# Optimization experiments

Measured on AMD Instinct MI355X. Metric: run time of the kernel, lower is better.

## Reference

```python
import jax, jax.numpy as jnp
import numpy as np

H = 16  # num heads
DH = 64  # head dim


def setup_inputs() -> dict:
    key = jax.random.key(0)
    ks = jax.random.split(key, 9)
    d = 1024
    s = 0.02
    return {
        "hidden_states": jax.random.normal(ks[0], (16, 1024, d), jnp.float32),
        "Wq": jax.random.normal(ks[1], (d, d), jnp.float32) * s,
        "bq": jax.random.normal(ks[2], (d,), jnp.float32) * s,
        "Wk": jax.random.normal(ks[3], (d, d), jnp.float32) * s,
        "bk": jax.random.normal(ks[4], (d,), jnp.float32) * s,
        "Wv": jax.random.normal(ks[5], (d, d), jnp.float32) * s,
        "bv": jax.random.normal(ks[6], (d,), jnp.float32) * s,
        "Wo": jax.random.normal(ks[7], (d, d), jnp.float32) * s,
        "bo": jax.random.normal(ks[8], (d,), jnp.float32) * s,
    }


def _heads(x):
    b, s, _ = x.shape
    return x.reshape(b, s, H, DH).transpose(0, 2, 1, 3)  # [B,H,S,Dh]


def reference(hidden_states, Wq, bq, Wk, bk, Wv, bv, Wo, bo):
    # torch nn.Linear: y = x @ W.T + b; weights here are [out, in]
    q = _heads(hidden_states @ Wq.T + bq)
    k = _heads(hidden_states @ Wk.T + bk)
    v = _heads(hidden_states @ Wv.T + bv)
    scores = jnp.einsum("bhqd,bhkd->bhqk", q, k) / jnp.sqrt(jnp.float32(DH))
    probs = jax.nn.softmax(scores, axis=-1)
    ctx = jnp.einsum("bhqk,bhkd->bhqd", probs, v)
    b, _, s, _ = ctx.shape
    ctx = ctx.transpose(0, 2, 1, 3).reshape(b, s, H * DH)
    out = ctx @ Wo.T + bo
    # module returns (attention_output, weights=None); return array only
    return out
```

## Files before the change

kernel.cpp:

```cpp
#include <hip/hip_runtime.h>
#include <hip/hip_bf16.h>
#include <stdint.h>


typedef short bf16x8 __attribute__((ext_vector_type(8)));
typedef float f32x4 __attribute__((ext_vector_type(4)));
typedef unsigned short ushort_t;
typedef ushort_t us8 __attribute__((ext_vector_type(8)));

__device__ __forceinline__ ushort_t f2b(float f) {
    unsigned x;
    __builtin_memcpy(&x, &f, 4);
    unsigned r = (x + 0x7fffu + ((x >> 16) & 1u)) >> 16;
    return (ushort_t)r;
}

__device__ __forceinline__ void glds16(const void* g, void* l) {
    __builtin_amdgcn_global_load_lds(
        (const __attribute__((address_space(1))) void*)g,
        (__attribute__((address_space(3))) void*)l, 16, 0, 0);
}

#define MFMA16(a, b, c) __builtin_amdgcn_mfma_f32_16x16x32_bf16((a), (b), (c), 0, 0, 0)

__global__ __launch_bounds__(256, 8) void cvt4_kernel(
    const float* __restrict__ s0, const float* __restrict__ s1,
    const float* __restrict__ s2, const float* __restrict__ s3,
    ushort_t* __restrict__ d0, ushort_t* __restrict__ d1,
    ushort_t* __restrict__ d2, ushort_t* __restrict__ d3, int n8)
{
    const float* in = (blockIdx.y == 0) ? s0 : (blockIdx.y == 1) ? s1
                       : (blockIdx.y == 2) ? s2 : s3;
    ushort_t* out = (blockIdx.y == 0) ? d0 : (blockIdx.y == 1) ? d1
                       : (blockIdx.y == 2) ? d2 : d3;
    int i = blockIdx.x * 256 + threadIdx.x;
    if (i >= n8) return;
    const float4* p = (const float4*)in + (size_t)i * 2;
    float4 a = p[0], b = p[1];
    us8 v;
    v[0] = f2b(a.x); v[1] = f2b(a.y); v[2] = f2b(a.z); v[3] = f2b(a.w);
    v[4] = f2b(b.x); v[5] = f2b(b.y); v[6] = f2b(b.z); v[7] = f2b(b.w);
    *((us8*)out + i) = v;
}

__global__ __launch_bounds__(256, 8) void cvt1_kernel(
    const float* __restrict__ in, ushort_t* __restrict__ out, int n8)
{
    int i = blockIdx.x * 256 + threadIdx.x;
    if (i >= n8) return;
    const float4* p = (const float4*)in + (size_t)i * 2;
    float4 a = p[0], b = p[1];
    us8 v;
    v[0] = f2b(a.x); v[1] = f2b(a.y); v[2] = f2b(a.z); v[3] = f2b(a.w);
    v[4] = f2b(b.x); v[5] = f2b(b.y); v[6] = f2b(b.z); v[7] = f2b(b.w);
    *((us8*)out + i) = v;
}

template <bool OUTF>
__global__ __launch_bounds__(512) void gemm256_kernel(
    const ushort_t* __restrict__ A,
    const ushort_t* __restrict__ W0, const ushort_t* __restrict__ W1, const ushort_t* __restrict__ W2,
    const float* __restrict__ b0, const float* __restrict__ b1, const float* __restrict__ b2,
    void* __restrict__ C0, void* __restrict__ C1, void* __restrict__ C2,
    float s0, float s1, float s2, int N, int K)
{
    const ushort_t* W = (blockIdx.z == 0) ? W0 : ((blockIdx.z == 1) ? W1 : W2);
    const float* bias = (blockIdx.z == 0) ? b0 : ((blockIdx.z == 1) ? b1 : b2);
    void* C = (blockIdx.z == 0) ? C0 : ((blockIdx.z == 1) ? C1 : C2);
    const float scale = (blockIdx.z == 0) ? s0 : ((blockIdx.z == 1) ? s1 : s2);

    __shared__ ushort_t lds[2][4][256 * 32];

    const int tid = threadIdx.x;
    const int lane = tid & 63;
    const int wave = tid >> 6;
    const int wr = wave >> 2;
    const int wc = wave & 3;
    const int rl = lane & 15;
    const int ck = lane >> 4;

    const int gx = gridDim.x;
    const int flat = blockIdx.y * gx + blockIdx.x;
    const int cpx = (gx * gridDim.y) >> 3;
    const int swz = (flat & 7) * cpx + (flat >> 3);
    const int bm = (swz % gx) * 256;
    const int bn = (swz / gx) * 256;

    const ushort_t* Ag = A + (size_t)bm * K;
    const ushort_t* Bg = W + (size_t)bn * K;

    const int q0 = tid, q1 = 512 + tid;
    const int sr0 = q0 >> 2, sc0 = (q0 & 3) * 8;
    const int sr1 = q1 >> 2, sc1 = (q1 & 3) * 8;

#define STG(gbase, kcol, dst) do { \
    glds16((gbase) + (size_t)sr0 * K + (kcol) + sc0, (dst) + q0 * 8); \
    glds16((gbase) + (size_t)sr1 * K + (kcol) + sc1, (dst) + q1 * 8); } while (0)

#define BARRIER() do { \
    __builtin_amdgcn_sched_barrier(0); \
    asm volatile("s_barrier" ::: "memory"); \
    __builtin_amdgcn_sched_barrier(0); } while (0)

#define VMCNT(n) asm volatile("s_waitcnt vmcnt(" #n ")" ::: "memory")

    f32x4 acc[8][4] = {};
    bf16x8 af[8], bfr[2];

    const int aoff = (wr * 128 + rl) * 32 + ck * 8;
    const int boff = (wc * 64 + rl) * 32 + ck * 8;

#define LDA(buf, kh) do { _Pragma("unroll") \
    for (int mi = 0; mi < 8; ++mi) \
        af[mi] = *(const bf16x8*)(&lds[buf][kh][0] + aoff + mi * 512); } while (0)
#define LDB(buf, kh, nb) do { \
    bfr[0] = *(const bf16x8*)(&lds[buf][2 + (kh)][0] + boff + (nb) * 1024); \
    bfr[1] = *(const bf16x8*)(&lds[buf][2 + (kh)][0] + boff + (nb) * 1024 + 512); } while (0)
#define MM(nb) do { __builtin_amdgcn_s_setprio(1); _Pragma("unroll") \
    for (int mi = 0; mi < 8; ++mi) { \
        acc[mi][2*(nb)]   = MFMA16(af[mi], bfr[0], acc[mi][2*(nb)]); \
        acc[mi][2*(nb)+1] = MFMA16(af[mi], bfr[1], acc[mi][2*(nb)+1]); } \
    __builtin_amdgcn_s_setprio(0); } while (0)

    STG(Ag, 0,  &lds[0][0][0]);
    STG(Bg, 0,  &lds[0][2][0]);
    STG(Ag, 32, &lds[0][1][0]);
    STG(Bg, 32, &lds[0][3][0]);
    STG(Ag, 64, &lds[1][0][0]);
    STG(Bg, 64, &lds[1][2][0]);
    VMCNT(4);
    BARRIER();

#pragma unroll 1
    for (int i = 0; i < 7; ++i) {
        const int t = 2 * i;
        const int kc1 = (t + 1) * 64, kc2 = (t + 2) * 64, kc3 = (t + 3) * 64;
        LDA(0, 0); LDB(0, 0, 0);
        STG(Ag, kc1 + 32, &lds[1][1][0]);
        BARRIER(); MM(0); BARRIER();
        LDB(0, 0, 1);
        STG(Bg, kc1 + 32, &lds[1][3][0]);
        BARRIER(); MM(1); BARRIER();
        LDA(0, 1); LDB(0, 1, 0);
        STG(Ag, kc2, &lds[0][0][0]);
        BARRIER(); MM(0); BARRIER();
        LDB(0, 1, 1);
        STG(Bg, kc2, &lds[0][2][0]);
        VMCNT(4);
        BARRIER(); MM(1); BARRIER();
        LDA(1, 0); LDB(1, 0, 0);
        STG(Ag, kc2 + 32, &lds[0][1][0]);
        BARRIER(); MM(0); BARRIER();
        LDB(1, 0, 1);
        STG(Bg, kc2 + 32, &lds[0][3][0]);
        BARRIER(); MM(1); BARRIER();
        LDA(1, 1); LDB(1, 1, 0);
        STG(Ag, kc3, &lds[1][0][0]);
        BARRIER(); MM(0); BARRIER();
        LDB(1, 1, 1);
        STG(Bg, kc3, &lds[1][2][0]);
        VMCNT(4);
        BARRIER(); MM(1); BARRIER();
    }

    {
        const int kc15 = 15 * 64;
        LDA(0, 0); LDB(0, 0, 0);
        STG(Ag, kc15 + 32, &lds[1][1][0]);
        BARRIER(); MM(0); BARRIER();
        LDB(0, 0, 1);
        STG(Bg, kc15 + 32, &lds[1][3][0]);
        BARRIER(); MM(1); BARRIER();
        LDA(0, 1); LDB(0, 1, 0);
        BARRIER(); MM(0); BARRIER();
        LDB(0, 1, 1);
        VMCNT(0);
        BARRIER(); MM(1); BARRIER();
        LDA(1, 0); LDB(1, 0, 0); MM(0);
        LDB(1, 0, 1); MM(1);
        LDA(1, 1); LDB(1, 1, 0); MM(0);
        LDB(1, 1, 1); MM(1);
    }

#pragma unroll
    for (int ni = 0; ni < 4; ++ni) {
        const int col = bn + wc * 64 + ni * 16 + rl;
        const float bv = bias[col];
#pragma unroll
        for (int mi = 0; mi < 8; ++mi) {
            const int rbase = bm + wr * 128 + mi * 16 + ck * 4;
#pragma unroll
            for (int r = 0; r < 4; ++r) {
                float v = (acc[mi][ni][r] + bv) * scale;
                if (OUTF)
                    ((float*)C)[(size_t)(rbase + r) * N + col] = v;
                else
                    ((ushort_t*)C)[(size_t)(rbase + r) * N + col] = f2b(v);
            }
        }
    }
#undef STG
#undef BARRIER
#undef VMCNT
#undef LDA
#undef LDB
#undef MM
}

__global__ __launch_bounds__(256, 4) void transpose_v_kernel(
    const ushort_t* __restrict__ V, ushort_t* __restrict__ Vt)
{
    __shared__ ushort_t t[64 * 65];
    const int bh = blockIdx.x;
    const int st = blockIdx.y;
    const int b = bh >> 4, h = bh & 15;
    const int tid = threadIdx.x;

#pragma unroll
    for (int i = 0; i < 16; ++i) {
        int e = i * 256 + tid;
        int s = e >> 6, d = e & 63;
        t[s * 65 + d] = V[(size_t)(b * 1024 + st * 64 + s) * 1024 + h * 64 + d];
    }
    __syncthreads();
#pragma unroll
    for (int i = 0; i < 16; ++i) {
        int e = i * 256 + tid;
        int d = e >> 6, s = e & 63;
        Vt[(size_t)(bh * 64 + d) * 1024 + st * 64 + s] = t[s * 65 + d];
    }
}

__global__ __launch_bounds__(256, 2) void attn_kernel(
    const ushort_t* __restrict__ Q, const ushort_t* __restrict__ K,
    const ushort_t* __restrict__ Vt, ushort_t* __restrict__ ctx)
{
    __shared__ ushort_t Ks[2][64 * 64];
    __shared__ ushort_t Vs[2][64 * 64];
    __shared__ ushort_t Ps[4][32 * 72];

    const int bh = blockIdx.x;
    const int qt = blockIdx.y;
    const int b = bh >> 4, h = bh & 15;
    const int tid = threadIdx.x;
    const int lane = tid & 63;
    const int wave = tid >> 6;
    const int q = lane >> 4;
    const int ml = lane & 15;

    const int cid0 = tid;
    const int cid1 = 256 + tid;
    const int r0 = cid0 >> 3, sc0 = (cid0 & 7) ^ (r0 & 7);
    const int r1 = cid1 >> 3, sc1 = (cid1 & 7) ^ (r1 & 7);
    const ushort_t* Kbase = K + (size_t)(b * 1024) * 1024 + h * 64;
    const ushort_t* Vbase = Vt + (size_t)(bh * 64) * 1024;

    bf16x8 qf[2][2];
#pragma unroll
    for (int mg = 0; mg < 2; ++mg) {
        int row = b * 1024 + qt * 128 + wave * 32 + mg * 16 + ml;
        const ushort_t* qp = Q + (size_t)row * 1024 + h * 64;
        qf[mg][0] = *(const bf16x8*)(qp + q * 8);
        qf[mg][1] = *(const bf16x8*)(qp + 32 + q * 8);
    }

    bf16x8 ones;
#pragma unroll
    for (int i = 0; i < 8; ++i) ones[i] = (short)0x3F80;

    f32x4 o[2][4] = {};
    f32x4 ls[2] = {};
    ushort_t* Pw = Ps[wave];

    glds16(Kbase + (size_t)r0 * 1024 + sc0 * 8, Ks[0] + cid0 * 8);
    glds16(Vbase + (size_t)r0 * 1024 + sc0 * 8, Vs[0] + cid0 * 8);
    glds16(Kbase + (size_t)r1 * 1024 + sc1 * 8, Ks[0] + cid1 * 8);
    glds16(Vbase + (size_t)r1 * 1024 + sc1 * 8, Vs[0] + cid1 * 8);

    for (int kt = 0; kt < 16; ++kt) {
        const int cur = kt & 1, nxt = cur ^ 1;
        __syncthreads();
        if (kt + 1 < 16) {
            const ushort_t* Kn = Kbase + (size_t)(kt + 1) * 64 * 1024;
            const ushort_t* Vn = Vbase + (kt + 1) * 64;
            glds16(Kn + (size_t)r0 * 1024 + sc0 * 8, Ks[nxt] + cid0 * 8);
            glds16(Vn + (size_t)r0 * 1024 + sc0 * 8, Vs[nxt] + cid0 * 8);
            glds16(Kn + (size_t)r1 * 1024 + sc1 * 8, Ks[nxt] + cid1 * 8);
            glds16(Vn + (size_t)r1 * 1024 + sc1 * 8, Vs[nxt] + cid1 * 8);
        }
        const ushort_t* Kc = Ks[cur];
        const ushort_t* Vc = Vs[cur];

#pragma unroll
        for (int n = 0; n < 4; ++n) {
            int row = n * 16 + ml;
            int c0 = q ^ (row & 7);
            int c1 = (4 + q) ^ (row & 7);
            bf16x8 k0 = *(const bf16x8*)(Kc + row * 64 + c0 * 8);
            bf16x8 k1 = *(const bf16x8*)(Kc + row * 64 + c1 * 8);
#pragma unroll
            for (int mg = 0; mg < 2; ++mg) {
                f32x4 z = {};
                z = MFMA16(k0, qf[mg][0], z);
                z = MFMA16(k1, qf[mg][1], z);
                float p0 = __builtin_amdgcn_exp2f(z[0]);
                float p1 = __builtin_amdgcn_exp2f(z[1]);
                float p2 = __builtin_amdgcn_exp2f(z[2]);
                float p3 = __builtin_amdgcn_exp2f(z[3]);
                __hip_bfloat162 h01 = __float22bfloat162_rn(make_float2(p0, p1));
                __hip_bfloat162 h23 = __float22bfloat162_rn(make_float2(p2, p3));
                uint2 dd;
                __builtin_memcpy(&dd.x, &h01, 4);
                __builtin_memcpy(&dd.y, &h23, 4);
                *(uint2*)(Pw + (mg * 16 + ml) * 72 + n * 16 + q * 4) = dd;
            }
        }

#pragma unroll
        for (int mg = 0; mg < 2; ++mg) {
            bf16x8 pf0 = *(const bf16x8*)(Pw + (mg * 16 + ml) * 72 + q * 8);
            bf16x8 pf1 = *(const bf16x8*)(Pw + (mg * 16 + ml) * 72 + 32 + q * 8);
            ls[mg] = MFMA16(pf0, ones, ls[mg]);
            ls[mg] = MFMA16(pf1, ones, ls[mg]);
#pragma unroll
            for (int n = 0; n < 4; ++n) {
                int row = n * 16 + ml;
                int c0 = q ^ (row & 7);
                int c1 = (4 + q) ^ (row & 7);
                bf16x8 v0 = *(const bf16x8*)(Vc + row * 64 + c0 * 8);
                bf16x8 v1 = *(const bf16x8*)(Vc + row * 64 + c1 * 8);
                o[mg][n] = MFMA16(pf0, v0, o[mg][n]);
                o[mg][n] = MFMA16(pf1, v1, o[mg][n]);
            }
        }
    }

    const int orow_base = b * 1024 + qt * 128 + wave * 32;
#pragma unroll
    for (int mg = 0; mg < 2; ++mg) {
#pragma unroll
        for (int r = 0; r < 4; ++r) {
            float lv = 1.0f / ls[mg][r];
            int orow = orow_base + mg * 16 + q * 4 + r;
#pragma unroll
            for (int n = 0; n < 4; ++n) {
                ctx[(size_t)orow * 1024 + h * 64 + n * 16 + ml] =
                    f2b(o[mg][n][r] * lv);
            }
        }
    }
}

extern "C" void kernel_launch(void* const* d_in, const int* in_sizes, int n_in,
                              void* d_out, int out_size, void* d_ws, size_t ws_size,
                              hipStream_t stream)
{
    const float* X  = (const float*)d_in[0];
    const float* Wq = (const float*)d_in[1];
    const float* bq = (const float*)d_in[2];
    const float* Wk = (const float*)d_in[3];
    const float* bk = (const float*)d_in[4];
    const float* Wv = (const float*)d_in[5];
    const float* bv = (const float*)d_in[6];
    const float* Wo = (const float*)d_in[7];
    const float* bo = (const float*)d_in[8];

    const int D = 1024;
    const int M = in_sizes[0] / D;
    const int Bb = M / 1024;
    const size_t MD = (size_t)M * D;
    const size_t DD = (size_t)D * D;

    ushort_t* ws  = (ushort_t*)d_ws;
    ushort_t* Xbf = ws;
    ushort_t* Qb  = ws + MD;
    ushort_t* Kb  = ws + 2 * MD;
    ushort_t* Vb  = ws + 3 * MD;
    ushort_t* Wqb = ws + 4 * MD;
    ushort_t* Wkb = Wqb + DD;
    ushort_t* Wvb = Wkb + DD;
    ushort_t* Wob = Wvb + DD;
    ushort_t* Vtb = Xbf;
    ushort_t* ctx = Vb;

    dim3 blk(256);
    dim3 blk512(512);

    cvt1_kernel<<<(int)(MD / 8 / 256), blk, 0, stream>>>(X, Xbf, (int)(MD / 8));
    cvt4_kernel<<<dim3((int)(DD / 8 / 256), 4), blk, 0, stream>>>(
        Wq, Wk, Wv, Wo, Wqb, Wkb, Wvb, Wob, (int)(DD / 8));

    const float qscale = 1.4426950408889634f * 0.125f;
    dim3 gqkv(M / 256, D / 256, 3);
    gemm256_kernel<false><<<gqkv, blk512, 0, stream>>>(Xbf, Wqb, Wkb, Wvb,
                                                       bq, bk, bv,
                                                       Qb, Kb, Vb,
                                                       qscale, 1.0f, 1.0f, D, D);

    transpose_v_kernel<<<dim3(Bb * 16, 16), blk, 0, stream>>>(Vb, Vtb);

    attn_kernel<<<dim3(Bb * 16, 8), blk, 0, stream>>>(Qb, Kb, Vtb, ctx);

    dim3 go(M / 256, D / 256, 1);
    gemm256_kernel<true><<<go, blk512, 0, stream>>>(ctx, Wob, Wob, Wob,
                                                    bo, bo, bo,
                                                    d_out, d_out, d_out,
                                                    1.0f, 1.0f, 1.0f, D, D);
}
```

Baseline: 412.1 us.

## Switch projection GEMM to 32x32x16 MFMA with rotated LDS layout and fewer barriers

```diff
diff --git a/kernel.cpp b/kernel.cpp
--- a/kernel.cpp
+++ b/kernel.cpp
@@ -5,6 +5,7 @@
 
 typedef short bf16x8 __attribute__((ext_vector_type(8)));
 typedef float f32x4 __attribute__((ext_vector_type(4)));
+typedef float f32x16 __attribute__((ext_vector_type(16)));
 typedef unsigned short ushort_t;
 typedef ushort_t us8 __attribute__((ext_vector_type(8)));
 
@@ -22,6 +23,7 @@
 }
 
 #define MFMA16(a, b, c) __builtin_amdgcn_mfma_f32_16x16x32_bf16((a), (b), (c), 0, 0, 0)
+#define MFMA32(a, b, c) __builtin_amdgcn_mfma_f32_32x32x16_bf16((a), (b), (c), 0, 0, 0)
 
 __global__ __launch_bounds__(256, 8) void cvt4_kernel(
     const float* __restrict__ s0, const float* __restrict__ s1,
@@ -76,8 +78,8 @@
     const int wave = tid >> 6;
     const int wr = wave >> 2;
     const int wc = wave & 3;
-    const int rl = lane & 15;
-    const int ck = lane >> 4;
+    const int r32 = lane & 31;
+    const int g = lane >> 5;
 
     const int gx = gridDim.x;
     const int flat = blockIdx.y * gx + blockIdx.x;
@@ -90,8 +92,8 @@
     const ushort_t* Bg = W + (size_t)bn * K;
 
     const int q0 = tid, q1 = 512 + tid;
-    const int sr0 = q0 >> 2, sc0 = (q0 & 3) * 8;
-    const int sr1 = q1 >> 2, sc1 = (q1 & 3) * 8;
+    const int sr0 = q0 >> 2, sc0 = (((q0 & 3) - (sr0 >> 1)) & 3) * 8;
+    const int sr1 = q1 >> 2, sc1 = (((q1 & 3) - (sr1 >> 1)) & 3) * 8;
 
 #define STG(gbase, kcol, dst) do { \
     glds16((gbase) + (size_t)sr0 * K + (kcol) + sc0, (dst) + q0 * 8); \
@@ -104,30 +106,37 @@
 
 #define VMCNT(n) asm volatile("s_waitcnt vmcnt(" #n ")" ::: "memory")
 
-    f32x4 acc[8][4] = {};
-    bf16x8 af[8], bfr[2];
-
-    const int aoff = (wr * 128 + rl) * 32 + ck * 8;
-    const int boff = (wc * 64 + rl) * 32 + ck * 8;
-
-#define LDA(buf, kh) do { _Pragma("unroll") \
-    for (int mi = 0; mi < 8; ++mi) \
-        af[mi] = *(const bf16x8*)(&lds[buf][kh][0] + aoff + mi * 512); } while (0)
-#define LDB(buf, kh, nb) do { \
-    bfr[0] = *(const bf16x8*)(&lds[buf][2 + (kh)][0] + boff + (nb) * 1024); \
-    bfr[1] = *(const bf16x8*)(&lds[buf][2 + (kh)][0] + boff + (nb) * 1024 + 512); } while (0)
-#define MM(nb) do { __builtin_amdgcn_s_setprio(1); _Pragma("unroll") \
-    for (int mi = 0; mi < 8; ++mi) { \
-        acc[mi][2*(nb)]   = MFMA16(af[mi], bfr[0], acc[mi][2*(nb)]); \
-        acc[mi][2*(nb)+1] = MFMA16(af[mi], bfr[1], acc[mi][2*(nb)+1]); } \
+#define ROT(r, c) (((((c) + ((r) >> 1)) & 3)) * 8)
+
+    f32x16 acc[4][2] = {};
+    bf16x8 af[2][2], bfr[2][2];
+
+#define LDA(buf, kh, mh) do { _Pragma("unroll") \
+    for (int i = 0; i < 2; ++i) { _Pragma("unroll") \
+        for (int t = 0; t < 2; ++t) { \
+            int row = wr * 128 + ((mh) * 2 + i) * 32 + r32; \
+            af[i][t] = *(const bf16x8*)(&lds[buf][kh][0] + row * 32 + ROT(row, 2 * t + g)); \
+        } } } while (0)
+#define LDB(buf, kh) do { _Pragma("unroll") \
+    for (int ni = 0; ni < 2; ++ni) { _Pragma("unroll") \
+        for (int t = 0; t < 2; ++t) { \
+            int row = wc * 64 + ni * 32 + r32; \
+            bfr[ni][t] = *(const bf16x8*)(&lds[buf][2 + (kh)][0] + row * 32 + ROT(row, 2 * t + g)); \
+        } } } while (0)
+#define MM(mh) do { __builtin_amdgcn_s_setprio(1); _Pragma("unroll") \
+    for (int i = 0; i < 2; ++i) { _Pragma("unroll") \
+        for (int ni = 0; ni < 2; ++ni) { \
+            acc[(mh) * 2 + i][ni] = MFMA32(af[i][0], bfr[ni][0], acc[(mh) * 2 + i][ni]); \
+            acc[(mh) * 2 + i][ni] = MFMA32(af[i][1], bfr[ni][1], acc[(mh) * 2 + i][ni]); \
+        } } \
     __builtin_amdgcn_s_setprio(0); } while (0)
 
     STG(Ag, 0,  &lds[0][0][0]);
     STG(Bg, 0,  &lds[0][2][0]);
     STG(Ag, 32, &lds[0][1][0]);
     STG(Bg, 32, &lds[0][3][0]);
+    STG(Bg, 64, &lds[1][2][0]);
     STG(Ag, 64, &lds[1][0][0]);
-    STG(Bg, 64, &lds[1][2][0]);
     VMCNT(4);
     BARRIER();
 
@@ -135,73 +144,78 @@
     for (int i = 0; i < 7; ++i) {
         const int t = 2 * i;
         const int kc1 = (t + 1) * 64, kc2 = (t + 2) * 64, kc3 = (t + 3) * 64;
-        LDA(0, 0); LDB(0, 0, 0);
+        LDB(0, 0); LDA(0, 0, 0);
+        STG(Bg, kc1 + 32, &lds[1][3][0]);
+        BARRIER(); MM(0);
+        LDA(0, 0, 1);
         STG(Ag, kc1 + 32, &lds[1][1][0]);
-        BARRIER(); MM(0); BARRIER();
-        LDB(0, 0, 1);
-        STG(Bg, kc1 + 32, &lds[1][3][0]);
-        BARRIER(); MM(1); BARRIER();
-        LDA(0, 1); LDB(0, 1, 0);
+        VMCNT(8);
+        BARRIER(); MM(1);
+        LDB(0, 1); LDA(0, 1, 0);
+        STG(Bg, kc2, &lds[0][2][0]);
+        BARRIER(); MM(0);
+        LDA(0, 1, 1);
         STG(Ag, kc2, &lds[0][0][0]);
-        BARRIER(); MM(0); BARRIER();
-        LDB(0, 1, 1);
-        STG(Bg, kc2, &lds[0][2][0]);
-        VMCNT(4);
-        BARRIER(); MM(1); BARRIER();
-        LDA(1, 0); LDB(1, 0, 0);
+        VMCNT(8);
+        BARRIER(); MM(1);
+        LDB(1, 0); LDA(1, 0, 0);
+        STG(Bg, kc2 + 32, &lds[0][3][0]);
+        BARRIER(); MM(0);
+        LDA(1, 0, 1);
         STG(Ag, kc2 + 32, &lds[0][1][0]);
-        BARRIER(); MM(0); BARRIER();
-        LDB(1, 0, 1);
-        STG(Bg, kc2 + 32, &lds[0][3][0]);
-        BARRIER(); MM(1); BARRIER();
-        LDA(1, 1); LDB(1, 1, 0);
+        VMCNT(8);
+        BARRIER(); MM(1);
+        LDB(1, 1); LDA(1, 1, 0);
+        STG(Bg, kc3, &lds[1][2][0]);
+        BARRIER(); MM(0);
+        LDA(1, 1, 1);
         STG(Ag, kc3, &lds[1][0][0]);
-        BARRIER(); MM(0); BARRIER();
-        LDB(1, 1, 1);
-        STG(Bg, kc3, &lds[1][2][0]);
-        VMCNT(4);
-        BARRIER(); MM(1); BARRIER();
+        VMCNT(8);
+        BARRIER(); MM(1);
     }
 
     {
         const int kc15 = 15 * 64;
-        LDA(0, 0); LDB(0, 0, 0);
+        LDB(0, 0); LDA(0, 0, 0);
+        STG(Bg, kc15 + 32, &lds[1][3][0]);
+        BARRIER(); MM(0);
+        LDA(0, 0, 1);
         STG(Ag, kc15 + 32, &lds[1][1][0]);
-        BARRIER(); MM(0); BARRIER();
-        LDB(0, 0, 1);
-        STG(Bg, kc15 + 32, &lds[1][3][0]);
-        BARRIER(); MM(1); BARRIER();
-        LDA(0, 1); LDB(0, 1, 0);
-        BARRIER(); MM(0); BARRIER();
-        LDB(0, 1, 1);
+        VMCNT(8);
+        BARRIER(); MM(1);
+        LDB(0, 1); LDA(0, 1, 0);
+        BARRIER(); MM(0);
+        LDA(0, 1, 1);
         VMCNT(0);
-        BARRIER(); MM(1); BARRIER();
-        LDA(1, 0); LDB(1, 0, 0); MM(0);
-        LDB(1, 0, 1); MM(1);
-        LDA(1, 1); LDB(1, 1, 0); MM(0);
-        LDB(1, 1, 1); MM(1);
-    }
-
-#pragma unroll
-    for (int ni = 0; ni < 4; ++ni) {
-        const int col = bn + wc * 64 + ni * 16 + rl;
+        BARRIER(); MM(1);
+        LDB(1, 0); LDA(1, 0, 0); MM(0);
+        LDA(1, 0, 1); MM(1);
+        LDB(1, 1); LDA(1, 1, 0); MM(0);
+        LDA(1, 1, 1); MM(1);
+    }
+
+#pragma unroll
+    for (int ni = 0; ni < 2; ++ni) {
+        const int col = bn + wc * 64 + ni * 32 + r32;
         const float bv = bias[col];
 #pragma unroll
-        for (int mi = 0; mi < 8; ++mi) {
-            const int rbase = bm + wr * 128 + mi * 16 + ck * 4;
-#pragma unroll
-            for (int r = 0; r < 4; ++r) {
-                float v = (acc[mi][ni][r] + bv) * scale;
+        for (int mi = 0; mi < 4; ++mi) {
+            const int rbase = bm + wr * 128 + mi * 32 + 4 * g;
+#pragma unroll
+            for (int reg = 0; reg < 16; ++reg) {
+                const int row = rbase + (reg & 3) + 8 * (reg >> 2);
+                float v = (acc[mi][ni][reg] + bv) * scale;
                 if (OUTF)
-                    ((float*)C)[(size_t)(rbase + r) * N + col] = v;
+                    ((float*)C)[(size_t)row * N + col] = v;
                 else
-                    ((ushort_t*)C)[(size_t)(rbase + r) * N + col] = f2b(v);
+                    ((ushort_t*)C)[(size_t)row * N + col] = f2b(v);
             }
         }
     }
 #undef STG
 #undef BARRIER
 #undef VMCNT
+#undef ROT
 #undef LDA
 #undef LDB
 #undef MM
```

New measurement: 398.7 us. 1.03x faster.
